# Kernel optimization log

Measured on AMD Instinct MI355X. Metric: run time of the kernel, lower is better.

The kernel has to match this reference:

```python
import jax, jax.numpy as jnp
import numpy as np

B, S, H, NH = 2, 2048, 1024, 16
HD = H // NH


def setup_inputs() -> dict:
    key = jax.random.key(0)
    ks = jax.random.split(key, 12)
    inp = {
        "query": jax.random.normal(ks[0], (B, S, H), dtype=jnp.float32),
        "key": jax.random.normal(ks[1], (B, S, H), dtype=jnp.float32),
        "value": jax.random.normal(ks[2], (B, S, H), dtype=jnp.float32),
        "mask": jnp.ones((B, 1, S, S), dtype=jnp.int32),
        "script_mask": jax.random.uniform(ks[3], (B, S, S), dtype=jnp.float32),
    }
    scale = 1.0 / np.sqrt(H)
    inp["Wq"] = jax.random.normal(ks[4], (H, H), dtype=jnp.float32) * scale
    inp["bq"] = jnp.zeros((H,), dtype=jnp.float32)
    inp["Wk"] = jax.random.normal(ks[5], (H, H), dtype=jnp.float32) * scale
    inp["bk"] = jnp.zeros((H,), dtype=jnp.float32)
    inp["Wv"] = jax.random.normal(ks[6], (H, H), dtype=jnp.float32) * scale
    inp["bv"] = jnp.zeros((H,), dtype=jnp.float32)
    inp["Wo"] = jax.random.normal(ks[7], (H, H), dtype=jnp.float32) * scale
    inp["bo"] = jnp.zeros((H,), dtype=jnp.float32)
    return inp


def reference(query, key, value, mask, script_mask, Wq, bq, Wk, bk, Wv, bv, Wo, bo):
    b, s, h = query.shape
    # projections; torch Linear: x @ W.T + b
    q = (query @ Wq.T + bq).reshape(b, s, NH, HD).transpose(0, 2, 1, 3)  # [b,nh,s,hd]
    k = (key @ Wk.T + bk).reshape(b, s, NH, HD).transpose(0, 2, 1, 3)
    v = (value @ Wv.T + bv).reshape(b, s, NH, HD).transpose(0, 2, 1, 3)
    scores = jnp.einsum("bhqd,bhkd->bhqk", q, k) / jnp.sqrt(jnp.float32(HD))
    # multiplicative script mask, broadcast over heads
    scores = scores * script_mask[:, None, :, :]
    # additive mask: positions where mask == 0 -> -inf
    scores = jnp.where(mask == 0, -jnp.inf, scores)
    attn = jax.nn.softmax(scores, axis=-1)
    out = jnp.einsum("bhqk,bhkd->bhqd", attn, v)  # [b,nh,s,hd]
    out = out.transpose(0, 2, 1, 3).reshape(b, s, h)
    return out @ Wo.T + bo
```

## Files before the change

kernel.cpp:

```cpp
#include <hip/hip_runtime.h>
#include <stdint.h>

#define NH 16
#define SEQ 2048
#define HDIM 1024

typedef short bf16x8 __attribute__((ext_vector_type(8)));
typedef float f32x4 __attribute__((ext_vector_type(4)));

#define NEG_BIG (-1.0e30f)

static __device__ __forceinline__ float bf2f(uint32_t u) {
  union { uint32_t u; float f; } v; v.u = u << 16; return v.f;
}
static __device__ __forceinline__ uint16_t f2bf(float f) {
  uint32_t u = __builtin_bit_cast(uint32_t, f);
  return (uint16_t)((u + 0x7FFFu + ((u >> 16) & 1u)) >> 16);
}
static __device__ __forceinline__ uint32_t pack2bf(float a, float b) {
  return (uint32_t)f2bf(a) | ((uint32_t)f2bf(b) << 16);
}

struct CvtArgs {
  const float* src[7];
  uint16_t* dst[7];
  int nblk[7];
};
__global__ __launch_bounds__(256) void cvt_bf16(CvtArgs a) {
  int ten = blockIdx.y;
  if (blockIdx.x >= a.nblk[ten]) return;
  size_t idx = ((size_t)blockIdx.x * 256 + threadIdx.x) * 8;
  const float* s = a.src[ten] + idx;
  float4 f0 = *(const float4*)(s);
  float4 f1 = *(const float4*)(s + 4);
  uint4 o;
  o.x = pack2bf(f0.x, f0.y);
  o.y = pack2bf(f0.z, f0.w);
  o.z = pack2bf(f1.x, f1.y);
  o.w = pack2bf(f1.z, f1.w);
  *(uint4*)(a.dst[ten] + idx) = o;
}

__global__ __launch_bounds__(256) void cm_prep(const int4* __restrict__ mask,
                                               const float4* __restrict__ sm,
                                               uint4* __restrict__ cm) {
  int i = blockIdx.x * 256 + threadIdx.x;
  int4 m0 = mask[2 * i];
  int4 m1 = mask[2 * i + 1];
  float4 s0 = sm[2 * i];
  float4 s1 = sm[2 * i + 1];
  const float c = 0.18033688011112042f;
  auto pk = [&](int mA, int mB, float fa, float fb) -> uint32_t {
    uint32_t o0 = mA ? (uint32_t)f2bf(fa * c) : 0xBF80u;
    uint32_t o1 = mB ? (uint32_t)f2bf(fb * c) : 0xBF80u;
    return o0 | (o1 << 16);
  };
  uint4 o;
  o.x = pk(m0.x, m0.y, s0.x, s0.y);
  o.y = pk(m0.z, m0.w, s0.z, s0.w);
  o.z = pk(m1.x, m1.y, s1.x, s1.y);
  o.w = pk(m1.z, m1.w, s1.z, s1.w);
  cm[i] = o;
}

struct GemmArgs {
  const uint16_t* A[4];
  const uint16_t* B[4];
  const float* bias[4];
  void* C[4];
};

#define LDA 40

__global__ __launch_bounds__(256) void gemm_bt(GemmArgs ga, int modeBase) {
  int mode = modeBase + blockIdx.y;
  const uint16_t* __restrict__ A = ga.A[mode];
  const uint16_t* __restrict__ Bm = ga.B[mode];
  const float* __restrict__ bias = ga.bias[mode];

  int bid = blockIdx.x;
  int tm, tn;
  if (mode == 2) { tm = bid & 7; tn = bid >> 3; }
  else           { tm = bid >> 3; tn = bid & 7; }

  __shared__ uint16_t As[128 * LDA];
  __shared__ uint16_t Bs[128 * LDA];

  int t = threadIdx.x;
  int lane = t & 63, w = t >> 6;
  int quad = lane >> 4, lm = lane & 15;
  int wm = w >> 1, wn = w & 1;

  const uint16_t* Ab = A + (size_t)tm * 128 * 1024;
  const uint16_t* Bb = Bm + (size_t)tn * 128 * 1024;
  int srow = w * 32 + (lane >> 2);
  int scol = (lane & 3) * 8;

  f32x4 acc[4][4] = {};

  for (int kk = 0; kk < 1024; kk += 32) {
    uint4 a0 = *(const uint4*)(Ab + (size_t)srow * 1024 + kk + scol);
    uint4 a1 = *(const uint4*)(Ab + (size_t)(srow + 16) * 1024 + kk + scol);
    uint4 b0 = *(const uint4*)(Bb + (size_t)srow * 1024 + kk + scol);
    uint4 b1 = *(const uint4*)(Bb + (size_t)(srow + 16) * 1024 + kk + scol);
    __syncthreads();
    *(uint4*)&As[srow * LDA + scol] = a0;
    *(uint4*)&As[(srow + 16) * LDA + scol] = a1;
    *(uint4*)&Bs[srow * LDA + scol] = b0;
    *(uint4*)&Bs[(srow + 16) * LDA + scol] = b1;
    __syncthreads();

    bf16x8 af[4], bfr[4];
#pragma unroll
    for (int i = 0; i < 4; i++)
      af[i] = *(const bf16x8*)&As[(wm * 64 + i * 16 + lm) * LDA + quad * 8];
#pragma unroll
    for (int j = 0; j < 4; j++)
      bfr[j] = *(const bf16x8*)&Bs[(wn * 64 + j * 16 + lm) * LDA + quad * 8];
#pragma unroll
    for (int i = 0; i < 4; i++)
#pragma unroll
      for (int j = 0; j < 4; j++)
        acc[i][j] = __builtin_amdgcn_mfma_f32_16x16x32_bf16(af[i], bfr[j], acc[i][j], 0, 0, 0);
  }

  int rowb = tm * 128 + wm * 64;
  int colb = tn * 128 + wn * 64;
#pragma unroll
  for (int i = 0; i < 4; i++) {
#pragma unroll
    for (int j = 0; j < 4; j++) {
      int col = colb + j * 16 + lm;
#pragma unroll
      for (int r = 0; r < 4; r++) {
        int row = rowb + i * 16 + quad * 4 + r;
        float v = acc[i][j][r];
        if (mode == 2) {
          v += bias[row];
          int hh = row >> 6, hd = row & 63, b = col >> 11, s2 = col & 2047;
          ((uint16_t*)ga.C[2])[((size_t)((b * NH + hh) * 64 + hd) << 11) + s2] = f2bf(v);
        } else if (mode == 3) {
          v += bias[col];
          ((float*)ga.C[3])[(size_t)row * 1024 + col] = v;
        } else {
          v += bias[col];
          int b = row >> 11, s2 = row & 2047, hh = col >> 6, hd = col & 63;
          ((uint16_t*)ga.C[mode])[(((size_t)(b * NH + hh) * 2048 + s2) << 6) + hd] = f2bf(v);
        }
      }
    }
  }
}

#define LDK 72

__global__ __launch_bounds__(256) void attn(const uint16_t* __restrict__ qp,
                                            const uint16_t* __restrict__ kp,
                                            const uint16_t* __restrict__ vt,
                                            const uint16_t* __restrict__ cm,
                                            uint16_t* __restrict__ ao) {
  int h = blockIdx.x, qt = blockIdx.y, b = blockIdx.z;
  int t = threadIdx.x;
  int lane = t & 63, w = t >> 6;
  int quad = lane >> 4, c = lane & 15;

  __shared__ uint16_t Ks[64 * LDK];
  __shared__ uint16_t VTs[64 * LDK];
  __shared__ uint16_t CMs[64 * LDK];
  __shared__ uint16_t Ps[64 * LDK];

  size_t bh = (size_t)(b * NH + h);
  const uint16_t* Kb = kp + bh * (SEQ * 64);
  const uint16_t* Vb = vt + bh * (64 * SEQ);
  const uint16_t* CMb = cm + ((size_t)b * SEQ + qt * 64) * SEQ;

  int qrow = qt * 64 + w * 16 + c;
  const uint16_t* Qb = qp + bh * (SEQ * 64) + (size_t)qrow * 64;
  bf16x8 qf0 = *(const bf16x8*)(Qb + quad * 8);
  bf16x8 qf1 = *(const bf16x8*)(Qb + 32 + quad * 8);

  f32x4 Oacc[4] = {};
  float m_run = NEG_BIG;
  float l_run = 0.0f;

  int krow = w * 8 + (lane >> 3);
  int kc = (lane & 7) * 8;
  int cr0 = t >> 3, cseg = (t & 7) * 8;

  for (int kt = 0; kt < SEQ; kt += 64) {
    uint4 k0 = *(const uint4*)(Kb + (size_t)(kt + krow) * 64 + kc);
    uint4 k1 = *(const uint4*)(Kb + (size_t)(kt + 32 + krow) * 64 + kc);
    uint4 v0g = *(const uint4*)(Vb + (size_t)krow * SEQ + kt + kc);
    uint4 v1g = *(const uint4*)(Vb + (size_t)(32 + krow) * SEQ + kt + kc);
    uint4 c0 = *(const uint4*)(CMb + (size_t)cr0 * SEQ + kt + cseg);
    uint4 c1 = *(const uint4*)(CMb + (size_t)(cr0 + 32) * SEQ + kt + cseg);
    __syncthreads();
    *(uint4*)&Ks[krow * LDK + kc] = k0;
    *(uint4*)&Ks[(krow + 32) * LDK + kc] = k1;
    *(uint4*)&VTs[krow * LDK + kc] = v0g;
    *(uint4*)&VTs[(krow + 32) * LDK + kc] = v1g;
    *(uint4*)&CMs[cr0 * LDK + cseg] = c0;
    *(uint4*)&CMs[(cr0 + 32) * LDK + cseg] = c1;
    __syncthreads();

    f32x4 st[4];
#pragma unroll
    for (int i = 0; i < 4; i++) {
      bf16x8 a0 = *(const bf16x8*)&Ks[(i * 16 + c) * LDK + quad * 8];
      bf16x8 a1 = *(const bf16x8*)&Ks[(i * 16 + c) * LDK + 32 + quad * 8];
      f32x4 z = {};
      z = __builtin_amdgcn_mfma_f32_16x16x32_bf16(a0, qf0, z, 0, 0, 0);
      st[i] = __builtin_amdgcn_mfma_f32_16x16x32_bf16(a1, qf1, z, 0, 0, 0);
    }

    float p[16];
    float tmax = NEG_BIG;
#pragma unroll
    for (int i = 0; i < 4; i++) {
      ushort4 cmv = *(const ushort4*)&CMs[(w * 16 + c) * LDK + i * 16 + quad * 4];
      const uint16_t* cmp_ = (const uint16_t*)&cmv;
#pragma unroll
      for (int r = 0; r < 4; r++) {
        float cf = bf2f(cmp_[r]);
        float sv = st[i][r] * cf;
        sv = (cf < 0.0f) ? NEG_BIG : sv;
        p[i * 4 + r] = sv;
        tmax = fmaxf(tmax, sv);
      }
    }
    tmax = fmaxf(tmax, __shfl_xor(tmax, 16));
    tmax = fmaxf(tmax, __shfl_xor(tmax, 32));
    float m_new = fmaxf(m_run, tmax);
    float alpha = exp2f(m_run - m_new);
    m_run = m_new;
    float ls = 0.0f;
#pragma unroll
    for (int z2 = 0; z2 < 16; z2++) {
      p[z2] = exp2f(p[z2] - m_new);
      ls += p[z2];
    }
    l_run = l_run * alpha + ls;
#pragma unroll
    for (int i = 0; i < 4; i++) Oacc[i] *= alpha;

#pragma unroll
    for (int i = 0; i < 4; i++) {
      uint2 pkd;
      pkd.x = pack2bf(p[i * 4 + 0], p[i * 4 + 1]);
      pkd.y = pack2bf(p[i * 4 + 2], p[i * 4 + 3]);
      *(uint2*)&Ps[(w * 16 + c) * LDK + i * 16 + quad * 4] = pkd;
    }
    __syncthreads();

    bf16x8 pf0 = *(const bf16x8*)&Ps[(w * 16 + c) * LDK + quad * 8];
    bf16x8 pf1 = *(const bf16x8*)&Ps[(w * 16 + c) * LDK + 32 + quad * 8];
#pragma unroll
    for (int i = 0; i < 4; i++) {
      bf16x8 v0 = *(const bf16x8*)&VTs[(i * 16 + c) * LDK + quad * 8];
      bf16x8 v1 = *(const bf16x8*)&VTs[(i * 16 + c) * LDK + 32 + quad * 8];
      Oacc[i] = __builtin_amdgcn_mfma_f32_16x16x32_bf16(v0, pf0, Oacc[i], 0, 0, 0);
      Oacc[i] = __builtin_amdgcn_mfma_f32_16x16x32_bf16(v1, pf1, Oacc[i], 0, 0, 0);
    }
  }

  float lf = l_run + __shfl_xor(l_run, 16);
  lf = lf + __shfl_xor(lf, 32);
  float inv = 1.0f / lf;
  uint16_t* Ob = ao + ((size_t)(b * SEQ) + qt * 64 + w * 16 + c) * HDIM + h * 64;
#pragma unroll
  for (int i = 0; i < 4; i++) {
    ushort4 ov;
    ov.x = f2bf(Oacc[i][0] * inv);
    ov.y = f2bf(Oacc[i][1] * inv);
    ov.z = f2bf(Oacc[i][2] * inv);
    ov.w = f2bf(Oacc[i][3] * inv);
    *(ushort4*)(Ob + i * 16 + quad * 4) = ov;
  }
}

extern "C" void kernel_launch(void* const* d_in, const int* in_sizes, int n_in,
                              void* d_out, int out_size, void* d_ws, size_t ws_size,
                              hipStream_t stream) {
  (void)in_sizes; (void)n_in; (void)out_size; (void)ws_size;
  const float* query = (const float*)d_in[0];
  const float* key   = (const float*)d_in[1];
  const float* value = (const float*)d_in[2];
  const int*   mask  = (const int*)d_in[3];
  const float* smask = (const float*)d_in[4];
  const float* Wq = (const float*)d_in[5];
  const float* bq = (const float*)d_in[6];
  const float* Wk = (const float*)d_in[7];
  const float* bk = (const float*)d_in[8];
  const float* Wv = (const float*)d_in[9];
  const float* bv = (const float*)d_in[10];
  const float* Wo = (const float*)d_in[11];
  const float* bo = (const float*)d_in[12];

  char* p = (char*)d_ws;
  uint16_t* xq  = (uint16_t*)p; p += (size_t)2 * SEQ * HDIM * 2;
  uint16_t* xk  = (uint16_t*)p; p += (size_t)2 * SEQ * HDIM * 2;
  uint16_t* xv  = (uint16_t*)p; p += (size_t)2 * SEQ * HDIM * 2;
  uint16_t* wqb = (uint16_t*)p; p += (size_t)HDIM * HDIM * 2;
  uint16_t* wkb = (uint16_t*)p; p += (size_t)HDIM * HDIM * 2;
  uint16_t* wvb = (uint16_t*)p; p += (size_t)HDIM * HDIM * 2;
  uint16_t* wob = (uint16_t*)p; p += (size_t)HDIM * HDIM * 2;
  uint16_t* qp  = (uint16_t*)p; p += (size_t)2 * NH * SEQ * 64 * 2;
  uint16_t* kpp = (uint16_t*)p; p += (size_t)2 * NH * SEQ * 64 * 2;
  uint16_t* vtp = (uint16_t*)p; p += (size_t)2 * NH * SEQ * 64 * 2;
  uint16_t* cmw = (uint16_t*)p; p += (size_t)2 * SEQ * SEQ * 2;
  uint16_t* aob = (uint16_t*)p; p += (size_t)2 * SEQ * HDIM * 2;

  CvtArgs ca;
  ca.src[0] = query; ca.dst[0] = xq;  ca.nblk[0] = 2048;
  ca.src[1] = key;   ca.dst[1] = xk;  ca.nblk[1] = 2048;
  ca.src[2] = value; ca.dst[2] = xv;  ca.nblk[2] = 2048;
  ca.src[3] = Wq;    ca.dst[3] = wqb; ca.nblk[3] = 512;
  ca.src[4] = Wk;    ca.dst[4] = wkb; ca.nblk[4] = 512;
  ca.src[5] = Wv;    ca.dst[5] = wvb; ca.nblk[5] = 512;
  ca.src[6] = Wo;    ca.dst[6] = wob; ca.nblk[6] = 512;
  cvt_bf16<<<dim3(2048, 7), 256, 0, stream>>>(ca);

  cm_prep<<<4096, 256, 0, stream>>>((const int4*)mask, (const float4*)smask, (uint4*)cmw);

  GemmArgs ga;
  ga.A[0] = xq;  ga.B[0] = wqb; ga.bias[0] = bq; ga.C[0] = qp;
  ga.A[1] = xk;  ga.B[1] = wkb; ga.bias[1] = bk; ga.C[1] = kpp;
  ga.A[2] = wvb; ga.B[2] = xv;  ga.bias[2] = bv; ga.C[2] = vtp;
  ga.A[3] = aob; ga.B[3] = wob; ga.bias[3] = bo; ga.C[3] = d_out;

  gemm_bt<<<dim3(256, 3), 256, 0, stream>>>(ga, 0);
  attn<<<dim3(NH, SEQ / 64, 2), 256, 0, stream>>>(qp, kpp, vtp, cmw, aob);
  gemm_bt<<<dim3(256, 1), 256, 0, stream>>>(ga, 3);
}
```

Measured before the change: 384.8 us.

## Load mask directly to registers, use hardware bf16 pack, lazy rescale, drop barrier

```diff
diff --git a/kernel.cpp b/kernel.cpp
--- a/kernel.cpp
+++ b/kernel.cpp
@@ -10,15 +10,13 @@
 
 #define NEG_BIG (-1.0e30f)
 
-static __device__ __forceinline__ float bf2f(uint32_t u) {
-  union { uint32_t u; float f; } v; v.u = u << 16; return v.f;
+static __device__ __forceinline__ uint32_t cvtpk_bf16(float lo, float hi) {
+  uint32_t r;
+  asm("v_cvt_pk_bf16_f32 %0, %1, %2" : "=v"(r) : "v"(lo), "v"(hi));
+  return r;
 }
 static __device__ __forceinline__ uint16_t f2bf(float f) {
-  uint32_t u = __builtin_bit_cast(uint32_t, f);
-  return (uint16_t)((u + 0x7FFFu + ((u >> 16) & 1u)) >> 16);
-}
-static __device__ __forceinline__ uint32_t pack2bf(float a, float b) {
-  return (uint32_t)f2bf(a) | ((uint32_t)f2bf(b) << 16);
+  return (uint16_t)cvtpk_bf16(f, f);
 }
 
 struct CvtArgs {
@@ -34,10 +32,10 @@
   float4 f0 = *(const float4*)(s);
   float4 f1 = *(const float4*)(s + 4);
   uint4 o;
-  o.x = pack2bf(f0.x, f0.y);
-  o.y = pack2bf(f0.z, f0.w);
-  o.z = pack2bf(f1.x, f1.y);
-  o.w = pack2bf(f1.z, f1.w);
+  o.x = cvtpk_bf16(f0.x, f0.y);
+  o.y = cvtpk_bf16(f0.z, f0.w);
+  o.z = cvtpk_bf16(f1.x, f1.y);
+  o.w = cvtpk_bf16(f1.z, f1.w);
   *(uint4*)(a.dst[ten] + idx) = o;
 }
 
@@ -49,11 +47,11 @@
   int4 m1 = mask[2 * i + 1];
   float4 s0 = sm[2 * i];
   float4 s1 = sm[2 * i + 1];
-  const float c = 0.18033688011112042f;
+  const float cst = 0.18033688011112042f;
   auto pk = [&](int mA, int mB, float fa, float fb) -> uint32_t {
-    uint32_t o0 = mA ? (uint32_t)f2bf(fa * c) : 0xBF80u;
-    uint32_t o1 = mB ? (uint32_t)f2bf(fb * c) : 0xBF80u;
-    return o0 | (o1 << 16);
+    float a = mA ? fa * cst : -1.0f;
+    float b = mB ? fb * cst : -1.0f;
+    return cvtpk_bf16(a, b);
   };
   uint4 o;
   o.x = pk(m0.x, m0.y, s0.x, s0.y);
@@ -166,7 +164,6 @@
 
   __shared__ uint16_t Ks[64 * LDK];
   __shared__ uint16_t VTs[64 * LDK];
-  __shared__ uint16_t CMs[64 * LDK];
   __shared__ uint16_t Ps[64 * LDK];
 
   size_t bh = (size_t)(b * NH + h);
@@ -185,82 +182,112 @@
 
   int krow = w * 8 + (lane >> 3);
   int kc = (lane & 7) * 8;
-  int cr0 = t >> 3, cseg = (t & 7) * 8;
+
+  const uint16_t* pK0 = Kb + (size_t)krow * 64 + kc;
+  const uint16_t* pK1 = pK0 + 32 * 64;
+  const uint16_t* pV0 = Vb + (size_t)krow * SEQ + kc;
+  const uint16_t* pV1 = pV0 + (size_t)32 * SEQ;
+  const uint16_t* pCM = CMb + (size_t)(w * 16 + c) * SEQ + quad * 4;
+
+  uint16_t* sK0 = &Ks[krow * LDK + kc];
+  uint16_t* sK1 = sK0 + 32 * LDK;
+  uint16_t* sV0 = &VTs[krow * LDK + kc];
+  uint16_t* sV1 = sV0 + 32 * LDK;
+
+  const uint16_t* rK = &Ks[c * LDK];
+  const uint16_t* rV = &VTs[c * LDK];
+  uint16_t* sP = &Ps[(w * 16 + c) * LDK];
+  int qo = quad * 8;
 
   for (int kt = 0; kt < SEQ; kt += 64) {
-    uint4 k0 = *(const uint4*)(Kb + (size_t)(kt + krow) * 64 + kc);
-    uint4 k1 = *(const uint4*)(Kb + (size_t)(kt + 32 + krow) * 64 + kc);
-    uint4 v0g = *(const uint4*)(Vb + (size_t)krow * SEQ + kt + kc);
-    uint4 v1g = *(const uint4*)(Vb + (size_t)(32 + krow) * SEQ + kt + kc);
-    uint4 c0 = *(const uint4*)(CMb + (size_t)cr0 * SEQ + kt + cseg);
-    uint4 c1 = *(const uint4*)(CMb + (size_t)(cr0 + 32) * SEQ + kt + cseg);
+    uint2 cm0 = *(const uint2*)(pCM);
+    uint2 cm1 = *(const uint2*)(pCM + 16);
+    uint2 cm2 = *(const uint2*)(pCM + 32);
+    uint2 cm3 = *(const uint2*)(pCM + 48);
+    uint4 k0  = *(const uint4*)(pK0);
+    uint4 k1  = *(const uint4*)(pK1);
+    uint4 v0g = *(const uint4*)(pV0);
+    uint4 v1g = *(const uint4*)(pV1);
+    pCM += 64; pK0 += 64 * 64; pK1 += 64 * 64; pV0 += 64; pV1 += 64;
     __syncthreads();
-    *(uint4*)&Ks[krow * LDK + kc] = k0;
-    *(uint4*)&Ks[(krow + 32) * LDK + kc] = k1;
-    *(uint4*)&VTs[krow * LDK + kc] = v0g;
-    *(uint4*)&VTs[(krow + 32) * LDK + kc] = v1g;
-    *(uint4*)&CMs[cr0 * LDK + cseg] = c0;
-    *(uint4*)&CMs[(cr0 + 32) * LDK + cseg] = c1;
+    *(uint4*)sK0 = k0;
+    *(uint4*)sK1 = k1;
+    *(uint4*)sV0 = v0g;
+    *(uint4*)sV1 = v1g;
     __syncthreads();
 
     f32x4 st[4];
+    __builtin_amdgcn_s_setprio(1);
 #pragma unroll
     for (int i = 0; i < 4; i++) {
-      bf16x8 a0 = *(const bf16x8*)&Ks[(i * 16 + c) * LDK + quad * 8];
-      bf16x8 a1 = *(const bf16x8*)&Ks[(i * 16 + c) * LDK + 32 + quad * 8];
+      bf16x8 a0 = *(const bf16x8*)(rK + i * 16 * LDK + qo);
+      bf16x8 a1 = *(const bf16x8*)(rK + i * 16 * LDK + 32 + qo);
       f32x4 z = {};
       z = __builtin_amdgcn_mfma_f32_16x16x32_bf16(a0, qf0, z, 0, 0, 0);
       st[i] = __builtin_amdgcn_mfma_f32_16x16x32_bf16(a1, qf1, z, 0, 0, 0);
     }
+    __builtin_amdgcn_s_setprio(0);
 
     float p[16];
     float tmax = NEG_BIG;
+    uint2 cmv[4] = {cm0, cm1, cm2, cm3};
 #pragma unroll
     for (int i = 0; i < 4; i++) {
-      ushort4 cmv = *(const ushort4*)&CMs[(w * 16 + c) * LDK + i * 16 + quad * 4];
-      const uint16_t* cmp_ = (const uint16_t*)&cmv;
+      uint32_t w0 = cmv[i].x, w1 = cmv[i].y;
+      float cf[4];
+      cf[0] = __builtin_bit_cast(float, w0 << 16);
+      cf[1] = __builtin_bit_cast(float, w0 & 0xffff0000u);
+      cf[2] = __builtin_bit_cast(float, w1 << 16);
+      cf[3] = __builtin_bit_cast(float, w1 & 0xffff0000u);
 #pragma unroll
       for (int r = 0; r < 4; r++) {
-        float cf = bf2f(cmp_[r]);
-        float sv = st[i][r] * cf;
-        sv = (cf < 0.0f) ? NEG_BIG : sv;
+        float sv = st[i][r] * cf[r];
+        sv = (cf[r] < 0.0f) ? NEG_BIG : sv;
         p[i * 4 + r] = sv;
-        tmax = fmaxf(tmax, sv);
       }
+      tmax = fmaxf(tmax,
+                   fmaxf(fmaxf(p[i * 4 + 0], p[i * 4 + 1]),
+                         fmaxf(p[i * 4 + 2], p[i * 4 + 3])));
     }
     tmax = fmaxf(tmax, __shfl_xor(tmax, 16));
     tmax = fmaxf(tmax, __shfl_xor(tmax, 32));
-    float m_new = fmaxf(m_run, tmax);
-    float alpha = exp2f(m_run - m_new);
-    m_run = m_new;
+    if (!__all(tmax <= m_run + 8.0f)) {
+      float m_new = fmaxf(m_run, tmax);
+      float alpha = exp2f(m_run - m_new);
+      m_run = m_new;
+      l_run *= alpha;
+#pragma unroll
+      for (int i = 0; i < 4; i++) Oacc[i] *= alpha;
+    }
     float ls = 0.0f;
 #pragma unroll
     for (int z2 = 0; z2 < 16; z2++) {
-      p[z2] = exp2f(p[z2] - m_new);
+      p[z2] = exp2f(p[z2] - m_run);
       ls += p[z2];
     }
-    l_run = l_run * alpha + ls;
-#pragma unroll
-    for (int i = 0; i < 4; i++) Oacc[i] *= alpha;
+    l_run += ls;
 
 #pragma unroll
     for (int i = 0; i < 4; i++) {
       uint2 pkd;
-      pkd.x = pack2bf(p[i * 4 + 0], p[i * 4 + 1]);
-      pkd.y = pack2bf(p[i * 4 + 2], p[i * 4 + 3]);
-      *(uint2*)&Ps[(w * 16 + c) * LDK + i * 16 + quad * 4] = pkd;
-    }
-    __syncthreads();
-
-    bf16x8 pf0 = *(const bf16x8*)&Ps[(w * 16 + c) * LDK + quad * 8];
-    bf16x8 pf1 = *(const bf16x8*)&Ps[(w * 16 + c) * LDK + 32 + quad * 8];
+      pkd.x = cvtpk_bf16(p[i * 4 + 0], p[i * 4 + 1]);
+      pkd.y = cvtpk_bf16(p[i * 4 + 2], p[i * 4 + 3]);
+      *(uint2*)(sP + i * 16 + quad * 4) = pkd;
+    }
+    asm volatile("s_waitcnt lgkmcnt(0)" ::: "memory");
+    __builtin_amdgcn_sched_barrier(0);
+
+    bf16x8 pf0 = *(const bf16x8*)(sP + qo);
+    bf16x8 pf1 = *(const bf16x8*)(sP + 32 + qo);
+    __builtin_amdgcn_s_setprio(1);
 #pragma unroll
     for (int i = 0; i < 4; i++) {
-      bf16x8 v0 = *(const bf16x8*)&VTs[(i * 16 + c) * LDK + quad * 8];
-      bf16x8 v1 = *(const bf16x8*)&VTs[(i * 16 + c) * LDK + 32 + quad * 8];
+      bf16x8 v0 = *(const bf16x8*)(rV + i * 16 * LDK + qo);
+      bf16x8 v1 = *(const bf16x8*)(rV + i * 16 * LDK + 32 + qo);
       Oacc[i] = __builtin_amdgcn_mfma_f32_16x16x32_bf16(v0, pf0, Oacc[i], 0, 0, 0);
       Oacc[i] = __builtin_amdgcn_mfma_f32_16x16x32_bf16(v1, pf1, Oacc[i], 0, 0, 0);
     }
+    __builtin_amdgcn_s_setprio(0);
   }
 
   float lf = l_run + __shfl_xor(l_run, 16);
@@ -269,12 +296,10 @@
   uint16_t* Ob = ao + ((size_t)(b * SEQ) + qt * 64 + w * 16 + c) * HDIM + h * 64;
 #pragma unroll
   for (int i = 0; i < 4; i++) {
-    ushort4 ov;
-    ov.x = f2bf(Oacc[i][0] * inv);
-    ov.y = f2bf(Oacc[i][1] * inv);
-    ov.z = f2bf(Oacc[i][2] * inv);
-    ov.w = f2bf(Oacc[i][3] * inv);
-    *(ushort4*)(Ob + i * 16 + quad * 4) = ov;
+    uint2 ov;
+    ov.x = cvtpk_bf16(Oacc[i][0] * inv, Oacc[i][1] * inv);
+    ov.y = cvtpk_bf16(Oacc[i][2] * inv, Oacc[i][3] * inv);
+    *(uint2*)(Ob + i * 16 + quad * 4) = ov;
   }
 }
 
```

Measured after the change: 367.5 us. 1.05x faster.
